# Performance work log

Measured on AMD Instinct MI355X. Metric: run time of the kernel, lower is better.

The kernel has to match this reference:

```python
import jax, jax.numpy as jnp
import numpy as np

C, H, O, T, B = 15, 256, 512, 60, 1024


def setup_inputs() -> dict:
    key = jax.random.key(0)
    ks = jax.random.split(key, 8)
    s = 1.0 / np.sqrt(H)
    return {
        "x": jax.random.normal(ks[0], (B, H), dtype=jnp.float32),
        "cam": jax.random.randint(ks[1], (B,), 0, C, dtype=jnp.int32),
        "W_ih": jax.random.uniform(ks[2], (C, 3 * H, H), jnp.float32, -s, s),
        "W_hh": jax.random.uniform(ks[3], (C, 3 * H, H), jnp.float32, -s, s),
        "b_ih": jax.random.uniform(ks[4], (C, 3 * H), jnp.float32, -s, s),
        "b_hh": jax.random.uniform(ks[5], (C, 3 * H), jnp.float32, -s, s),
        "Wc": jax.random.uniform(ks[6], (C, O, H), jnp.float32, -s, s),
        "bc": jax.random.uniform(ks[7], (C, O), jnp.float32, -s, s),
    }


def reference(x, cam, W_ih, W_hh, b_ih, b_hh, Wc, bc):
    # Gather per-sample (per-camera) parameters once.
    Wi = W_ih[cam]          # [B, 3H, H]
    Wh = W_hh[cam]          # [B, 3H, H]
    bi = b_ih[cam]          # [B, 3H]
    bh = b_hh[cam]          # [B, 3H]
    Wcs = Wc[cam]           # [B, O, H]
    bcs = bc[cam]           # [B, O]

    # Input is constant across timesteps -> input gate preactivations computed once.
    gi = jnp.einsum('bh,bgh->bg', x, Wi) + bi   # [B, 3H]
    gi_r, gi_z, gi_n = jnp.split(gi, 3, axis=1)

    h0 = jnp.zeros_like(x)  # [B, H]

    def step(h, _):
        gh = jnp.einsum('bh,bgh->bg', h, Wh) + bh
        gh_r, gh_z, gh_n = jnp.split(gh, 3, axis=1)
        r = jax.nn.sigmoid(gi_r + gh_r)
        z = jax.nn.sigmoid(gi_z + gh_z)
        n = jnp.tanh(gi_n + r * gh_n)
        h_new = (1.0 - z) * n + z * h
        out = jax.nn.sigmoid(jnp.einsum('bh,boh->bo', h_new, Wcs) + bcs)  # [B, O]
        return h_new, out

    _, outs = jax.lax.scan(step, h0, None, length=T)  # [T, B, O]
    return jnp.transpose(outs, (1, 2, 0))             # [B, O, T]
```

## Files before the change

### kernel.cpp

```cpp
#include <hip/hip_runtime.h>
#include <hip/hip_fp16.h>

#define C_    15
#define H_    256
#define O_    512
#define T_    60
#define B_    1024
#define G3H_  768
#define TS    16
#define MAXG  12
#define NSLOT 96
#define NU    80
#define TCH   10

typedef __attribute__((ext_vector_type(8))) short bf16x8;
typedef __attribute__((ext_vector_type(4))) float f32x4;

__device__ __forceinline__ unsigned short f2bf(float f) {
    union { float f; unsigned u; } v; v.f = f;
    return (unsigned short)((v.u + 0x7FFFu + ((v.u >> 16) & 1u)) >> 16);
}
__device__ __forceinline__ float sigf(float x) { return 1.f / (1.f + __expf(-x)); }

__global__ __launch_bounds__(256) void sort_kernel(const int* __restrict__ cam,
    int* __restrict__ order, int* __restrict__ tcam, int* __restrict__ toff,
    int* __restrict__ tcnt)
{
    __shared__ int cnt[C_], start[C_], fill[C_];
    int tid = threadIdx.x;
    if (tid < C_) cnt[tid] = 0;
    if (tid < NSLOT) { tcam[tid] = -1; toff[tid] = 0; tcnt[tid] = 0; }
    __syncthreads();
    for (int b = tid; b < B_; b += 256) atomicAdd(&cnt[cam[b]], 1);
    __syncthreads();
    if (tid == 0) {
        int run = 0;
        for (int c = 0; c < C_; ++c) { start[c] = run; fill[c] = run; run += cnt[c]; }
    }
    __syncthreads();
    for (int b = tid; b < B_; b += 256) {
        int pos = atomicAdd(&fill[cam[b]], 1);
        order[pos] = b;
    }
    __syncthreads();
    if (tid == 0) {
        int gcnt[8] = {0,0,0,0,0,0,0,0};
        for (int c = 0; c < C_; ++c) gcnt[c & 7] += (cnt[c] + TS - 1) / TS;
        int maxg = 0;
        for (int g = 0; g < 8; ++g) maxg = max(maxg, gcnt[g]);
        if (maxg <= MAXG) {
            for (int g = 0; g < 8; ++g) {
                int k = 0;
                for (int c = g; c < C_; c += 8)
                    for (int r = 0; r < cnt[c]; r += TS) {
                        int slot = g + 8 * k;
                        tcam[slot] = c; toff[slot] = start[c] + r;
                        tcnt[slot] = min(TS, cnt[c] - r); ++k;
                    }
            }
        } else {
            int ti = 0;
            for (int c = 0; c < C_; ++c)
                for (int r = 0; r < cnt[c]; r += TS) {
                    tcam[ti] = c; toff[ti] = start[c] + r;
                    tcnt[ti] = min(TS, cnt[c] - r); ++ti;
                }
        }
    }
}

__global__ __launch_bounds__(256) void cvt_kernel(const float* __restrict__ src,
    unsigned short* __restrict__ dst, int n4)
{
    int i = blockIdx.x * 256 + threadIdx.x;
    if (i < n4) {
        float4 v = ((const float4*)src)[i];
        unsigned p0 = (unsigned)f2bf(v.x) | ((unsigned)f2bf(v.y) << 16);
        unsigned p1 = (unsigned)f2bf(v.z) | ((unsigned)f2bf(v.w) << 16);
        ((uint2*)dst)[i] = make_uint2(p0, p1);
    }
}

__global__ __launch_bounds__(64) void pack_kernel(
    const float* __restrict__ Whh, const float* __restrict__ Wc,
    unsigned short* __restrict__ Wpack)
{
    int cu = blockIdx.x;
    int c = cu / NU, u = cu - c * NU;
    int lane = threadIdx.x, q = lane >> 4, l16 = lane & 15;
    const float* src = (u < 48)
        ? &Whh[((size_t)c * G3H_ + u * 16 + l16) * H_]
        : &Wc[((size_t)c * O_ + (u - 48) * 16 + l16) * H_];
    unsigned short* dst = Wpack + ((size_t)cu * 8) * 512 + lane * 8;
#pragma unroll
    for (int kk = 0; kk < 8; ++kk) {
        float4 v0 = *(const float4*)&src[kk * 32 + q * 8];
        float4 v1 = *(const float4*)&src[kk * 32 + q * 8 + 4];
        unsigned short* d = dst + kk * 512;
        d[0] = f2bf(v0.x); d[1] = f2bf(v0.y); d[2] = f2bf(v0.z); d[3] = f2bf(v0.w);
        d[4] = f2bf(v1.x); d[5] = f2bf(v1.y); d[6] = f2bf(v1.z); d[7] = f2bf(v1.w);
    }
}

__global__ __launch_bounds__(384) void gi_mfma(
    const float* __restrict__ x, const unsigned short* __restrict__ Wih_b,
    const float* __restrict__ bih, const float* __restrict__ bhh,
    const int* __restrict__ order, const int* __restrict__ tcam,
    const int* __restrict__ toff, const int* __restrict__ tcnt,
    float* __restrict__ gi)
{
    int c = tcam[blockIdx.x]; if (c < 0) return;
    int cnt = tcnt[blockIdx.x], off = toff[blockIdx.x];
    int tid = threadIdx.x;
    __shared__ unsigned short hbfs[TS * 264];
    for (int idx = tid; idx < TS * 64; idx += 384) {
        int m = idx >> 6, c4 = idx & 63;
        float4 v = make_float4(0.f, 0.f, 0.f, 0.f);
        if (m < cnt) v = *(const float4*)&x[(size_t)order[off + m] * H_ + (c4 << 2)];
        unsigned p0 = (unsigned)f2bf(v.x) | ((unsigned)f2bf(v.y) << 16);
        unsigned p1 = (unsigned)f2bf(v.z) | ((unsigned)f2bf(v.w) << 16);
        *(uint2*)&hbfs[m * 264 + (c4 << 2)] = make_uint2(p0, p1);
    }
    __syncthreads();
    int w = tid >> 6, lane = tid & 63, q = lane >> 4, l16 = lane & 15;
    f32x4 acc[2][4];
#pragma unroll
    for (int i = 0; i < 2; ++i)
#pragma unroll
        for (int nt = 0; nt < 4; ++nt) acc[i][nt] = (f32x4){0.f, 0.f, 0.f, 0.f};
    const unsigned short* bp[2];
#pragma unroll
    for (int i = 0; i < 2; ++i)
        bp[i] = Wih_b + ((size_t)c * G3H_ + (2 * w + i) * 64 + l16) * H_;
    const unsigned short* ap = &hbfs[l16 * 264 + q * 8];
#pragma unroll 2
    for (int kk = 0; kk < 8; ++kk) {
        bf16x8 a = *(const bf16x8*)(ap + kk * 32);
#pragma unroll
        for (int i = 0; i < 2; ++i)
#pragma unroll
            for (int nt = 0; nt < 4; ++nt) {
                bf16x8 b = *(const bf16x8*)(bp[i] + (size_t)nt * 16 * H_ + kk * 32 + q * 8);
                acc[i][nt] = __builtin_amdgcn_mfma_f32_16x16x32_bf16(a, b, acc[i][nt], 0, 0, 0);
            }
    }
#pragma unroll
    for (int i = 0; i < 2; ++i) {
        int u = 2 * w + i;
#pragma unroll
        for (int nt = 0; nt < 4; ++nt) {
            int col = u * 64 + nt * 16 + l16;
            float bias = bih[c * G3H_ + col] + (col < 2 * H_ ? bhh[c * G3H_ + col] : 0.f);
#pragma unroll
            for (int r = 0; r < 4; ++r) {
                int m = q * 4 + r;
                gi[((size_t)(blockIdx.x * TS + m)) * G3H_ + col] = acc[i][nt][r] + bias;
            }
        }
    }
}

__global__ __launch_bounds__(512, 2) void persist_kernel(
    const unsigned short* __restrict__ Wpack, const float* __restrict__ bhh,
    const float* __restrict__ gi, const int* __restrict__ tcam,
    unsigned short* __restrict__ htraj)
{
    int slot = blockIdx.x;
    int c = tcam[slot]; if (c < 0) return;
    int tid = threadIdx.x, w = tid >> 6, lane = tid & 63, q = lane >> 4, l16 = lane & 15;

    __shared__ float gisT[G3H_][20];
    __shared__ unsigned short hbf[2][16][264];

    for (int idx = tid; idx < TS * G3H_; idx += 512) {
        int m = idx / G3H_, col = idx - m * G3H_;
        gisT[col][m] = gi[((size_t)(slot * TS + m)) * G3H_ + col];
    }

    bf16x8 wf[6][8];
#pragma unroll
    for (int ii = 0; ii < 3; ++ii)
#pragma unroll
        for (int jj = 0; jj < 2; ++jj)
#pragma unroll
            for (int kk = 0; kk < 8; ++kk)
                wf[ii * 2 + jj][kk] = *(const bf16x8*)(
                    Wpack + (((size_t)(c * NU + ii * 16 + w + 8 * jj)) * 8 + kk) * 512 + lane * 8);

    float bhn[2], hreg[2][4];
#pragma unroll
    for (int i = 0; i < 2; ++i) {
        int col = (w + 8 * i) * 16 + l16;
        bhn[i] = bhh[c * G3H_ + 2 * H_ + col];
#pragma unroll
        for (int r = 0; r < 4; ++r) hreg[i][r] = 0.f;
    }
    unsigned short* hp = htraj + ((size_t)slot * TS + q * 4) * 256 + w * 16 + l16;
    __syncthreads();

#pragma unroll 2
    for (int s = 0; s < T_; ++s) {
        int wbuf = s & 1, rbuf = wbuf ^ 1;
        f32x4 acc[6];
#pragma unroll
        for (int ui = 0; ui < 6; ++ui) acc[ui] = (f32x4){0.f, 0.f, 0.f, 0.f};
        if (s > 0) {
#pragma unroll
            for (int kk = 0; kk < 8; ++kk) {
                bf16x8 a = *(const bf16x8*)&hbf[rbuf][l16][kk * 32 + q * 8];
#pragma unroll
                for (int ui = 0; ui < 6; ++ui)
                    acc[ui] = __builtin_amdgcn_mfma_f32_16x16x32_bf16(a, wf[ui][kk], acc[ui], 0, 0, 0);
            }
        }
#pragma unroll
        for (int i = 0; i < 2; ++i) {
            int col = (w + 8 * i) * 16 + l16;
            f32x4 gr = *(const f32x4*)&gisT[col][q * 4];
            f32x4 gz = *(const f32x4*)&gisT[H_ + col][q * 4];
            f32x4 gn = *(const f32x4*)&gisT[2 * H_ + col][q * 4];
#pragma unroll
            for (int r = 0; r < 4; ++r) {
                float rr = sigf(gr[r] + acc[i][r]);
                float zz = sigf(gz[r] + acc[2 + i][r]);
                float pre = gn[r] + rr * (acc[4 + i][r] + bhn[i]);
                float nn = 2.f * sigf(2.f * pre) - 1.f;
                float hn = (1.f - zz) * nn + zz * hreg[i][r];
                hreg[i][r] = hn;
                unsigned short hb = f2bf(hn);
                hbf[wbuf][q * 4 + r][col] = hb;
                hp[r * 256 + i * 128] = hb;
            }
        }
        hp += (size_t)NSLOT * TS * 256;
        asm volatile("s_waitcnt lgkmcnt(0)" ::: "memory");
        __builtin_amdgcn_s_barrier();
        __builtin_amdgcn_sched_barrier(0);
    }
}

__global__ __launch_bounds__(512, 2) void out_kernel(
    const unsigned short* __restrict__ Wpack, const float* __restrict__ bc,
    const unsigned short* __restrict__ htraj, const int* __restrict__ order,
    const int* __restrict__ tcam, const int* __restrict__ toff,
    const int* __restrict__ tcnt, unsigned short* __restrict__ outT,
    int direct, float* __restrict__ outp)
{
    int slot = blockIdx.x;
    int c = tcam[slot]; if (c < 0) return;
    int n = tcnt[slot], off = toff[slot];
    int tid = threadIdx.x, w = tid >> 6, lane = tid & 63, q = lane >> 4, l16 = lane & 15;
    __shared__ unsigned short hb[2][16][264];
    __shared__ int ord16[16];
    if (tid < 16) ord16[tid] = (tid < n) ? order[off + tid] : -1;

    bf16x8 wf[4][8];
    const unsigned short* wb = Wpack + ((size_t)c * NU + 48 + w * 4) * 8 * 512 + lane * 8;
#pragma unroll
    for (int ui = 0; ui < 4; ++ui)
#pragma unroll
        for (int kk = 0; kk < 8; ++kk)
            wf[ui][kk] = *(const bf16x8*)(wb + ((size_t)ui * 8 + kk) * 512);
    float bcr[4];
#pragma unroll
    for (int ui = 0; ui < 4; ++ui)
        bcr[ui] = bc[c * O_ + (w * 4 + ui) * 16 + l16];

    int m = tid >> 5, c8 = (tid & 31) * 8;
    const unsigned short* hsrc =
        &htraj[(((size_t)(blockIdx.y * TCH) * NSLOT + slot) * 16 + m) * 256 + c8];
    uint4 stg = *(const uint4*)hsrc;
    *(uint4*)&hb[0][m][c8] = stg;
    __syncthreads();

    for (int ti = 0; ti < TCH; ++ti) {
        int t = blockIdx.y * TCH + ti;
        int cur = ti & 1;
        if (ti + 1 < TCH)
            stg = *(const uint4*)(hsrc + (size_t)(ti + 1) * NSLOT * TS * 256);
        f32x4 acc[4];
#pragma unroll
        for (int ui = 0; ui < 4; ++ui) acc[ui] = (f32x4){0.f, 0.f, 0.f, 0.f};
#pragma unroll
        for (int kk = 0; kk < 8; ++kk) {
            bf16x8 a = *(const bf16x8*)&hb[cur][l16][kk * 32 + q * 8];
#pragma unroll
            for (int ui = 0; ui < 4; ++ui)
                acc[ui] = __builtin_amdgcn_mfma_f32_16x16x32_bf16(a, wf[ui][kk], acc[ui], 0, 0, 0);
        }
#pragma unroll
        for (int ui = 0; ui < 4; ++ui) {
            int o = (w * 4 + ui) * 16 + l16;
#pragma unroll
            for (int r = 0; r < 4; ++r) {
                int b = ord16[q * 4 + r];
                if (b >= 0) {
                    float val = sigf(acc[ui][r] + bcr[ui]);
                    if (direct) outp[((size_t)b * O_ + o) * T_ + t] = val;
                    else outT[((size_t)t * B_ + b) * O_ + o] =
                             __half_as_ushort(__float2half_rn(val));
                }
            }
        }
        if (ti + 1 < TCH) {
            *(uint4*)&hb[cur ^ 1][m][c8] = stg;
            asm volatile("s_waitcnt lgkmcnt(0)" ::: "memory");
            __builtin_amdgcn_s_barrier();
            __builtin_amdgcn_sched_barrier(0);
        }
    }
}

__global__ __launch_bounds__(256) void transpose_kernel(
    const unsigned short* __restrict__ outT, float* __restrict__ outp)
{
    int b = blockIdx.x, o0 = blockIdx.y * 64;
    __shared__ float ts[T_][65];
    int tid = threadIdx.x;
    for (int idx = tid; idx < T_ * 64; idx += 256) {
        int t = idx >> 6, o = idx & 63;
        ts[t][o] = __half2float(__ushort_as_half(outT[((size_t)t * B_ + b) * O_ + o0 + o]));
    }
    __syncthreads();
    for (int idx = tid; idx < 64 * T_; idx += 256) {
        int o = idx / T_, t = idx - o * T_;
        outp[((size_t)b * O_ + o0 + o) * T_ + t] = ts[t][o];
    }
}

extern "C" void kernel_launch(void* const* d_in, const int* in_sizes, int n_in,
                              void* d_out, int out_size, void* d_ws, size_t ws_size,
                              hipStream_t stream)
{
    const float* x   = (const float*)d_in[0];
    const int*   cam = (const int*)d_in[1];
    const float* Wih = (const float*)d_in[2];
    const float* Whh = (const float*)d_in[3];
    const float* bih = (const float*)d_in[4];
    const float* bhh = (const float*)d_in[5];
    const float* Wc  = (const float*)d_in[6];
    const float* bc  = (const float*)d_in[7];
    float* outp = (float*)d_out;

    char* w = (char*)d_ws;
    unsigned short* Wih_b = (unsigned short*)w; w += (size_t)C_ * G3H_ * H_ * 2;
    unsigned short* Wpack = (unsigned short*)w; w += (size_t)C_ * NU * 8 * 512 * 2;
    int* order = (int*)w; w += B_ * 4;
    int* tcam  = (int*)w; w += NSLOT * 4;
    int* toff  = (int*)w; w += NSLOT * 4;
    int* tcnt  = (int*)w; w += NSLOT * 4;
    float* gi  = (float*)w; w += (size_t)NSLOT * TS * G3H_ * 4;
    unsigned short* htraj = (unsigned short*)w; w += (size_t)T_ * NSLOT * 16 * 256 * 2;
    unsigned short* outT = (unsigned short*)w;
    size_t need = (size_t)(w - (char*)d_ws) + (size_t)T_ * B_ * O_ * 2;
    int direct = (ws_size < need) ? 1 : 0;

    sort_kernel<<<1, 256, 0, stream>>>(cam, order, tcam, toff, tcnt);
    cvt_kernel<<<(C_ * G3H_ * H_ / 4 + 255) / 256, 256, 0, stream>>>(Wih, Wih_b, C_ * G3H_ * H_ / 4);
    pack_kernel<<<C_ * NU, 64, 0, stream>>>(Whh, Wc, Wpack);
    gi_mfma<<<NSLOT, 384, 0, stream>>>(x, Wih_b, bih, bhh, order, tcam, toff, tcnt, gi);
    persist_kernel<<<NSLOT, 512, 0, stream>>>(Wpack, bhh, gi, tcam, htraj);
    out_kernel<<<dim3(NSLOT, T_ / TCH), 512, 0, stream>>>(Wpack, bc, htraj, order, tcam,
                                                          toff, tcnt, outT, direct, outp);
    if (!direct)
        transpose_kernel<<<dim3(B_, O_ / 64), 256, 0, stream>>>(outT, outp);
}
```

Before: 439.9 us.

## Fuse prep kernels and overlap GRU recurrence with output projection via flags

Merges the sort, weight-convert and weight-pack kernels into one prep launch. It also fuses the input-gate GEMM, the GRU recurrence and the output projection into one kernel, where producer blocks publish per-slot progress flags every TCH steps and consumer blocks spin on them to compute outputs while the recurrence continues. This removes several launches, the gi round trip through global memory, and the serialization between the recurrence and output stages. The risk is deadlock if consumer blocks are resident while producers are not, and 192 blocks at launch bound (512,1) with large shared usage may not all be co-resident.

```diff
diff --git a/kernel.cpp b/kernel.cpp
--- a/kernel.cpp
+++ b/kernel.cpp
@@ -10,7 +10,10 @@
 #define TS    16
 #define MAXG  12
 #define NSLOT 96
+#define NPROD 96
 #define NU    80
+#define PACKB 300
+#define CVTB  2880
 #define TCH   10
 
 typedef __attribute__((ext_vector_type(8))) short bf16x8;
@@ -22,291 +25,275 @@
 }
 __device__ __forceinline__ float sigf(float x) { return 1.f / (1.f + __expf(-x)); }
 
-__global__ __launch_bounds__(256) void sort_kernel(const int* __restrict__ cam,
+__global__ __launch_bounds__(256) void prep_kernel(
+    const int* __restrict__ cam, const float* __restrict__ Wih,
+    const float* __restrict__ Whh, const float* __restrict__ Wc,
     int* __restrict__ order, int* __restrict__ tcam, int* __restrict__ toff,
-    int* __restrict__ tcnt)
+    int* __restrict__ tcnt, int* __restrict__ flags,
+    unsigned short* __restrict__ Wih_b, unsigned short* __restrict__ Wpack)
 {
-    __shared__ int cnt[C_], start[C_], fill[C_];
-    int tid = threadIdx.x;
-    if (tid < C_) cnt[tid] = 0;
-    if (tid < NSLOT) { tcam[tid] = -1; toff[tid] = 0; tcnt[tid] = 0; }
-    __syncthreads();
-    for (int b = tid; b < B_; b += 256) atomicAdd(&cnt[cam[b]], 1);
-    __syncthreads();
-    if (tid == 0) {
-        int run = 0;
-        for (int c = 0; c < C_; ++c) { start[c] = run; fill[c] = run; run += cnt[c]; }
-    }
-    __syncthreads();
-    for (int b = tid; b < B_; b += 256) {
-        int pos = atomicAdd(&fill[cam[b]], 1);
-        order[pos] = b;
-    }
-    __syncthreads();
-    if (tid == 0) {
-        int gcnt[8] = {0,0,0,0,0,0,0,0};
-        for (int c = 0; c < C_; ++c) gcnt[c & 7] += (cnt[c] + TS - 1) / TS;
-        int maxg = 0;
-        for (int g = 0; g < 8; ++g) maxg = max(maxg, gcnt[g]);
-        if (maxg <= MAXG) {
-            for (int g = 0; g < 8; ++g) {
-                int k = 0;
-                for (int c = g; c < C_; c += 8)
+    int bid = blockIdx.x, tid = threadIdx.x;
+    if (bid == 0) {
+        __shared__ int cnt[C_], start[C_], fill[C_];
+        if (tid < C_) cnt[tid] = 0;
+        if (tid < NSLOT) { tcam[tid] = -1; toff[tid] = 0; tcnt[tid] = 0; flags[tid] = 0; }
+        __syncthreads();
+        for (int b = tid; b < B_; b += 256) atomicAdd(&cnt[cam[b]], 1);
+        __syncthreads();
+        if (tid == 0) {
+            int run = 0;
+            for (int c = 0; c < C_; ++c) { start[c] = run; fill[c] = run; run += cnt[c]; }
+        }
+        __syncthreads();
+        for (int b = tid; b < B_; b += 256) {
+            int pos = atomicAdd(&fill[cam[b]], 1);
+            order[pos] = b;
+        }
+        __syncthreads();
+        if (tid == 0) {
+            int gcnt[8] = {0,0,0,0,0,0,0,0};
+            for (int c = 0; c < C_; ++c) gcnt[c & 7] += (cnt[c] + TS - 1) / TS;
+            int maxg = 0;
+            for (int g = 0; g < 8; ++g) maxg = max(maxg, gcnt[g]);
+            if (maxg <= MAXG) {
+                for (int g = 0; g < 8; ++g) {
+                    int k = 0;
+                    for (int c = g; c < C_; c += 8)
+                        for (int r = 0; r < cnt[c]; r += TS) {
+                            int slot = g + 8 * k;
+                            tcam[slot] = c; toff[slot] = start[c] + r;
+                            tcnt[slot] = min(TS, cnt[c] - r); ++k;
+                        }
+                }
+            } else {
+                int ti = 0;
+                for (int c = 0; c < C_; ++c)
                     for (int r = 0; r < cnt[c]; r += TS) {
-                        int slot = g + 8 * k;
-                        tcam[slot] = c; toff[slot] = start[c] + r;
-                        tcnt[slot] = min(TS, cnt[c] - r); ++k;
+                        tcam[ti] = c; toff[ti] = start[c] + r;
+                        tcnt[ti] = min(TS, cnt[c] - r); ++ti;
                     }
             }
-        } else {
-            int ti = 0;
-            for (int c = 0; c < C_; ++c)
-                for (int r = 0; r < cnt[c]; r += TS) {
-                    tcam[ti] = c; toff[ti] = start[c] + r;
-                    tcnt[ti] = min(TS, cnt[c] - r); ++ti;
-                }
-        }
-    }
-}
-
-__global__ __launch_bounds__(256) void cvt_kernel(const float* __restrict__ src,
-    unsigned short* __restrict__ dst, int n4)
-{
-    int i = blockIdx.x * 256 + threadIdx.x;
-    if (i < n4) {
-        float4 v = ((const float4*)src)[i];
+        }
+    } else if (bid <= PACKB) {
+        int cu = (bid - 1) * 4 + (tid >> 6);
+        int c = cu / NU, u = cu - c * NU;
+        int lane = tid & 63, q = lane >> 4, l16 = lane & 15;
+        const float* src = (u < 48)
+            ? &Whh[((size_t)c * G3H_ + u * 16 + l16) * H_]
+            : &Wc[((size_t)c * O_ + (u - 48) * 16 + l16) * H_];
+        unsigned short* dst = Wpack + ((size_t)cu * 8) * 512 + lane * 8;
+#pragma unroll
+        for (int kk = 0; kk < 8; ++kk) {
+            float4 v0 = *(const float4*)&src[kk * 32 + q * 8];
+            float4 v1 = *(const float4*)&src[kk * 32 + q * 8 + 4];
+            unsigned short* d = dst + kk * 512;
+            d[0] = f2bf(v0.x); d[1] = f2bf(v0.y); d[2] = f2bf(v0.z); d[3] = f2bf(v0.w);
+            d[4] = f2bf(v1.x); d[5] = f2bf(v1.y); d[6] = f2bf(v1.z); d[7] = f2bf(v1.w);
+        }
+    } else {
+        int i = (bid - 1 - PACKB) * 256 + tid;
+        float4 v = ((const float4*)Wih)[i];
         unsigned p0 = (unsigned)f2bf(v.x) | ((unsigned)f2bf(v.y) << 16);
         unsigned p1 = (unsigned)f2bf(v.z) | ((unsigned)f2bf(v.w) << 16);
-        ((uint2*)dst)[i] = make_uint2(p0, p1);
+        ((uint2*)Wih_b)[i] = make_uint2(p0, p1);
     }
 }
 
-__global__ __launch_bounds__(64) void pack_kernel(
-    const float* __restrict__ Whh, const float* __restrict__ Wc,
-    unsigned short* __restrict__ Wpack)
-{
-    int cu = blockIdx.x;
-    int c = cu / NU, u = cu - c * NU;
-    int lane = threadIdx.x, q = lane >> 4, l16 = lane & 15;
-    const float* src = (u < 48)
-        ? &Whh[((size_t)c * G3H_ + u * 16 + l16) * H_]
-        : &Wc[((size_t)c * O_ + (u - 48) * 16 + l16) * H_];
-    unsigned short* dst = Wpack + ((size_t)cu * 8) * 512 + lane * 8;
-#pragma unroll
-    for (int kk = 0; kk < 8; ++kk) {
-        float4 v0 = *(const float4*)&src[kk * 32 + q * 8];
-        float4 v1 = *(const float4*)&src[kk * 32 + q * 8 + 4];
-        unsigned short* d = dst + kk * 512;
-        d[0] = f2bf(v0.x); d[1] = f2bf(v0.y); d[2] = f2bf(v0.z); d[3] = f2bf(v0.w);
-        d[4] = f2bf(v1.x); d[5] = f2bf(v1.y); d[6] = f2bf(v1.z); d[7] = f2bf(v1.w);
-    }
-}
-
-__global__ __launch_bounds__(384) void gi_mfma(
+__global__ __launch_bounds__(512, 1) void mega_kernel(
     const float* __restrict__ x, const unsigned short* __restrict__ Wih_b,
-    const float* __restrict__ bih, const float* __restrict__ bhh,
+    const unsigned short* __restrict__ Wpack, const float* __restrict__ bih,
+    const float* __restrict__ bhh, const float* __restrict__ bc,
     const int* __restrict__ order, const int* __restrict__ tcam,
     const int* __restrict__ toff, const int* __restrict__ tcnt,
-    float* __restrict__ gi)
+    int* __restrict__ flags, unsigned short* __restrict__ htraj,
+    unsigned short* __restrict__ outT, int direct, float* __restrict__ outp)
 {
-    int c = tcam[blockIdx.x]; if (c < 0) return;
-    int cnt = tcnt[blockIdx.x], off = toff[blockIdx.x];
-    int tid = threadIdx.x;
-    __shared__ unsigned short hbfs[TS * 264];
-    for (int idx = tid; idx < TS * 64; idx += 384) {
-        int m = idx >> 6, c4 = idx & 63;
-        float4 v = make_float4(0.f, 0.f, 0.f, 0.f);
-        if (m < cnt) v = *(const float4*)&x[(size_t)order[off + m] * H_ + (c4 << 2)];
-        unsigned p0 = (unsigned)f2bf(v.x) | ((unsigned)f2bf(v.y) << 16);
-        unsigned p1 = (unsigned)f2bf(v.z) | ((unsigned)f2bf(v.w) << 16);
-        *(uint2*)&hbfs[m * 264 + (c4 << 2)] = make_uint2(p0, p1);
-    }
-    __syncthreads();
+    int bid = blockIdx.x, tid = threadIdx.x;
     int w = tid >> 6, lane = tid & 63, q = lane >> 4, l16 = lane & 15;
-    f32x4 acc[2][4];
-#pragma unroll
-    for (int i = 0; i < 2; ++i)
-#pragma unroll
-        for (int nt = 0; nt < 4; ++nt) acc[i][nt] = (f32x4){0.f, 0.f, 0.f, 0.f};
-    const unsigned short* bp[2];
-#pragma unroll
-    for (int i = 0; i < 2; ++i)
-        bp[i] = Wih_b + ((size_t)c * G3H_ + (2 * w + i) * 64 + l16) * H_;
-    const unsigned short* ap = &hbfs[l16 * 264 + q * 8];
-#pragma unroll 2
-    for (int kk = 0; kk < 8; ++kk) {
-        bf16x8 a = *(const bf16x8*)(ap + kk * 32);
-#pragma unroll
-        for (int i = 0; i < 2; ++i)
-#pragma unroll
-            for (int nt = 0; nt < 4; ++nt) {
-                bf16x8 b = *(const bf16x8*)(bp[i] + (size_t)nt * 16 * H_ + kk * 32 + q * 8);
-                acc[i][nt] = __builtin_amdgcn_mfma_f32_16x16x32_bf16(a, b, acc[i][nt], 0, 0, 0);
-            }
-    }
-#pragma unroll
-    for (int i = 0; i < 2; ++i) {
-        int u = 2 * w + i;
-#pragma unroll
-        for (int nt = 0; nt < 4; ++nt) {
-            int col = u * 64 + nt * 16 + l16;
-            float bias = bih[c * G3H_ + col] + (col < 2 * H_ ? bhh[c * G3H_ + col] : 0.f);
-#pragma unroll
-            for (int r = 0; r < 4; ++r) {
-                int m = q * 4 + r;
-                gi[((size_t)(blockIdx.x * TS + m)) * G3H_ + col] = acc[i][nt][r] + bias;
-            }
-        }
-    }
-}
-
-__global__ __launch_bounds__(512, 2) void persist_kernel(
-    const unsigned short* __restrict__ Wpack, const float* __restrict__ bhh,
-    const float* __restrict__ gi, const int* __restrict__ tcam,
-    unsigned short* __restrict__ htraj)
-{
-    int slot = blockIdx.x;
-    int c = tcam[slot]; if (c < 0) return;
-    int tid = threadIdx.x, w = tid >> 6, lane = tid & 63, q = lane >> 4, l16 = lane & 15;
-
-    __shared__ float gisT[G3H_][20];
-    __shared__ unsigned short hbf[2][16][264];
-
-    for (int idx = tid; idx < TS * G3H_; idx += 512) {
-        int m = idx / G3H_, col = idx - m * G3H_;
-        gisT[col][m] = gi[((size_t)(slot * TS + m)) * G3H_ + col];
-    }
-
-    bf16x8 wf[6][8];
-#pragma unroll
-    for (int ii = 0; ii < 3; ++ii)
-#pragma unroll
-        for (int jj = 0; jj < 2; ++jj)
-#pragma unroll
-            for (int kk = 0; kk < 8; ++kk)
-                wf[ii * 2 + jj][kk] = *(const bf16x8*)(
-                    Wpack + (((size_t)(c * NU + ii * 16 + w + 8 * jj)) * 8 + kk) * 512 + lane * 8);
-
-    float bhn[2], hreg[2][4];
-#pragma unroll
-    for (int i = 0; i < 2; ++i) {
-        int col = (w + 8 * i) * 16 + l16;
-        bhn[i] = bhh[c * G3H_ + 2 * H_ + col];
-#pragma unroll
-        for (int r = 0; r < 4; ++r) hreg[i][r] = 0.f;
-    }
-    unsigned short* hp = htraj + ((size_t)slot * TS + q * 4) * 256 + w * 16 + l16;
-    __syncthreads();
-
-#pragma unroll 2
-    for (int s = 0; s < T_; ++s) {
-        int wbuf = s & 1, rbuf = wbuf ^ 1;
-        f32x4 acc[6];
-#pragma unroll
-        for (int ui = 0; ui < 6; ++ui) acc[ui] = (f32x4){0.f, 0.f, 0.f, 0.f};
-        if (s > 0) {
+
+    if (bid < NPROD) {
+        int slot = bid;
+        int c = tcam[slot]; if (c < 0) return;
+        int cnt = tcnt[slot], off = toff[slot];
+
+        __shared__ float gisT[G3H_][20];
+        __shared__ unsigned short hbf[2][16][264];
+
+        for (int idx = tid; idx < TS * 64; idx += 512) {
+            int m = idx >> 6, c4 = idx & 63;
+            float4 v = make_float4(0.f, 0.f, 0.f, 0.f);
+            if (m < cnt) v = *(const float4*)&x[(size_t)order[off + m] * H_ + (c4 << 2)];
+            unsigned p0 = (unsigned)f2bf(v.x) | ((unsigned)f2bf(v.y) << 16);
+            unsigned p1 = (unsigned)f2bf(v.z) | ((unsigned)f2bf(v.w) << 16);
+            *(uint2*)&hbf[0][m][c4 << 2] = make_uint2(p0, p1);
+        }
+        __syncthreads();
+
+        {
+            f32x4 acc[6];
+#pragma unroll
+            for (int ui = 0; ui < 6; ++ui) acc[ui] = (f32x4){0.f, 0.f, 0.f, 0.f};
 #pragma unroll
             for (int kk = 0; kk < 8; ++kk) {
-                bf16x8 a = *(const bf16x8*)&hbf[rbuf][l16][kk * 32 + q * 8];
-#pragma unroll
-                for (int ui = 0; ui < 6; ++ui)
-                    acc[ui] = __builtin_amdgcn_mfma_f32_16x16x32_bf16(a, wf[ui][kk], acc[ui], 0, 0, 0);
-            }
-        }
+                bf16x8 a = *(const bf16x8*)&hbf[0][l16][kk * 32 + q * 8];
+#pragma unroll
+                for (int ui = 0; ui < 6; ++ui) {
+                    int col = (w * 6 + ui) * 16 + l16;
+                    bf16x8 b = *(const bf16x8*)(Wih_b + ((size_t)c * G3H_ + col) * H_ + kk * 32 + q * 8);
+                    acc[ui] = __builtin_amdgcn_mfma_f32_16x16x32_bf16(a, b, acc[ui], 0, 0, 0);
+                }
+            }
+#pragma unroll
+            for (int ui = 0; ui < 6; ++ui) {
+                int col = (w * 6 + ui) * 16 + l16;
+                float bias = bih[c * G3H_ + col] + (col < 2 * H_ ? bhh[c * G3H_ + col] : 0.f);
+#pragma unroll
+                for (int r = 0; r < 4; ++r) gisT[col][q * 4 + r] = acc[ui][r] + bias;
+            }
+        }
+        __builtin_amdgcn_sched_barrier(0);
+
+        bf16x8 wf[6][8];
+#pragma unroll
+        for (int ii = 0; ii < 3; ++ii)
+#pragma unroll
+            for (int jj = 0; jj < 2; ++jj)
+#pragma unroll
+                for (int kk = 0; kk < 8; ++kk)
+                    wf[ii * 2 + jj][kk] = *(const bf16x8*)(
+                        Wpack + (((size_t)(c * NU + ii * 16 + w + 8 * jj)) * 8 + kk) * 512 + lane * 8);
+
+        float bhn[2], hreg[2][4];
 #pragma unroll
         for (int i = 0; i < 2; ++i) {
             int col = (w + 8 * i) * 16 + l16;
-            f32x4 gr = *(const f32x4*)&gisT[col][q * 4];
-            f32x4 gz = *(const f32x4*)&gisT[H_ + col][q * 4];
-            f32x4 gn = *(const f32x4*)&gisT[2 * H_ + col][q * 4];
-#pragma unroll
-            for (int r = 0; r < 4; ++r) {
-                float rr = sigf(gr[r] + acc[i][r]);
-                float zz = sigf(gz[r] + acc[2 + i][r]);
-                float pre = gn[r] + rr * (acc[4 + i][r] + bhn[i]);
-                float nn = 2.f * sigf(2.f * pre) - 1.f;
-                float hn = (1.f - zz) * nn + zz * hreg[i][r];
-                hreg[i][r] = hn;
-                unsigned short hb = f2bf(hn);
-                hbf[wbuf][q * 4 + r][col] = hb;
-                hp[r * 256 + i * 128] = hb;
-            }
-        }
-        hp += (size_t)NSLOT * TS * 256;
-        asm volatile("s_waitcnt lgkmcnt(0)" ::: "memory");
-        __builtin_amdgcn_s_barrier();
-        __builtin_amdgcn_sched_barrier(0);
-    }
-}
-
-__global__ __launch_bounds__(512, 2) void out_kernel(
-    const unsigned short* __restrict__ Wpack, const float* __restrict__ bc,
-    const unsigned short* __restrict__ htraj, const int* __restrict__ order,
-    const int* __restrict__ tcam, const int* __restrict__ toff,
-    const int* __restrict__ tcnt, unsigned short* __restrict__ outT,
-    int direct, float* __restrict__ outp)
-{
-    int slot = blockIdx.x;
-    int c = tcam[slot]; if (c < 0) return;
-    int n = tcnt[slot], off = toff[slot];
-    int tid = threadIdx.x, w = tid >> 6, lane = tid & 63, q = lane >> 4, l16 = lane & 15;
-    __shared__ unsigned short hb[2][16][264];
-    __shared__ int ord16[16];
-    if (tid < 16) ord16[tid] = (tid < n) ? order[off + tid] : -1;
-
-    bf16x8 wf[4][8];
-    const unsigned short* wb = Wpack + ((size_t)c * NU + 48 + w * 4) * 8 * 512 + lane * 8;
-#pragma unroll
-    for (int ui = 0; ui < 4; ++ui)
-#pragma unroll
-        for (int kk = 0; kk < 8; ++kk)
-            wf[ui][kk] = *(const bf16x8*)(wb + ((size_t)ui * 8 + kk) * 512);
-    float bcr[4];
-#pragma unroll
-    for (int ui = 0; ui < 4; ++ui)
-        bcr[ui] = bc[c * O_ + (w * 4 + ui) * 16 + l16];
-
-    int m = tid >> 5, c8 = (tid & 31) * 8;
-    const unsigned short* hsrc =
-        &htraj[(((size_t)(blockIdx.y * TCH) * NSLOT + slot) * 16 + m) * 256 + c8];
-    uint4 stg = *(const uint4*)hsrc;
-    *(uint4*)&hb[0][m][c8] = stg;
-    __syncthreads();
-
-    for (int ti = 0; ti < TCH; ++ti) {
-        int t = blockIdx.y * TCH + ti;
-        int cur = ti & 1;
-        if (ti + 1 < TCH)
-            stg = *(const uint4*)(hsrc + (size_t)(ti + 1) * NSLOT * TS * 256);
-        f32x4 acc[4];
-#pragma unroll
-        for (int ui = 0; ui < 4; ++ui) acc[ui] = (f32x4){0.f, 0.f, 0.f, 0.f};
-#pragma unroll
-        for (int kk = 0; kk < 8; ++kk) {
-            bf16x8 a = *(const bf16x8*)&hb[cur][l16][kk * 32 + q * 8];
-#pragma unroll
-            for (int ui = 0; ui < 4; ++ui)
-                acc[ui] = __builtin_amdgcn_mfma_f32_16x16x32_bf16(a, wf[ui][kk], acc[ui], 0, 0, 0);
-        }
-#pragma unroll
-        for (int ui = 0; ui < 4; ++ui) {
-            int o = (w * 4 + ui) * 16 + l16;
-#pragma unroll
-            for (int r = 0; r < 4; ++r) {
-                int b = ord16[q * 4 + r];
-                if (b >= 0) {
-                    float val = sigf(acc[ui][r] + bcr[ui]);
-                    if (direct) outp[((size_t)b * O_ + o) * T_ + t] = val;
-                    else outT[((size_t)t * B_ + b) * O_ + o] =
-                             __half_as_ushort(__float2half_rn(val));
-                }
-            }
-        }
-        if (ti + 1 < TCH) {
-            *(uint4*)&hb[cur ^ 1][m][c8] = stg;
+            bhn[i] = bhh[c * G3H_ + 2 * H_ + col];
+#pragma unroll
+            for (int r = 0; r < 4; ++r) hreg[i][r] = 0.f;
+        }
+        unsigned short* hp = htraj + ((size_t)slot * TS + q * 4) * 256 + w * 16 + l16;
+        __syncthreads();
+
+#pragma unroll 2
+        for (int s = 0; s < T_; ++s) {
+            int wbuf = s & 1, rbuf = wbuf ^ 1;
+            f32x4 acc[6];
+#pragma unroll
+            for (int ui = 0; ui < 6; ++ui) acc[ui] = (f32x4){0.f, 0.f, 0.f, 0.f};
+            if (s > 0) {
+#pragma unroll
+                for (int kk = 0; kk < 8; ++kk) {
+                    bf16x8 a = *(const bf16x8*)&hbf[rbuf][l16][kk * 32 + q * 8];
+#pragma unroll
+                    for (int ui = 0; ui < 6; ++ui)
+                        acc[ui] = __builtin_amdgcn_mfma_f32_16x16x32_bf16(a, wf[ui][kk], acc[ui], 0, 0, 0);
+                }
+            }
+#pragma unroll
+            for (int i = 0; i < 2; ++i) {
+                int col = (w + 8 * i) * 16 + l16;
+                f32x4 gr = *(const f32x4*)&gisT[col][q * 4];
+                f32x4 gz = *(const f32x4*)&gisT[H_ + col][q * 4];
+                f32x4 gn = *(const f32x4*)&gisT[2 * H_ + col][q * 4];
+#pragma unroll
+                for (int r = 0; r < 4; ++r) {
+                    float rr = sigf(gr[r] + acc[i][r]);
+                    float zz = sigf(gz[r] + acc[2 + i][r]);
+                    float pre = gn[r] + rr * (acc[4 + i][r] + bhn[i]);
+                    float nn = 2.f * sigf(2.f * pre) - 1.f;
+                    float hn = (1.f - zz) * nn + zz * hreg[i][r];
+                    hreg[i][r] = hn;
+                    unsigned short hb = f2bf(hn);
+                    hbf[wbuf][q * 4 + r][col] = hb;
+                    hp[r * 256 + i * 128] = hb;
+                }
+            }
+            hp += (size_t)NSLOT * TS * 256;
+            if (((s + 1) % TCH) == 0) {
+                __threadfence();
+                __syncthreads();
+                if (tid == 0)
+                    __hip_atomic_store(&flags[slot], s + 1, __ATOMIC_RELEASE,
+                                       __HIP_MEMORY_SCOPE_AGENT);
+            } else {
+                asm volatile("s_waitcnt lgkmcnt(0)" ::: "memory");
+                __builtin_amdgcn_s_barrier();
+                __builtin_amdgcn_sched_barrier(0);
+            }
+        }
+    } else {
+        int slot = bid - NPROD;
+        int c = tcam[slot]; if (c < 0) return;
+        int n = tcnt[slot], off = toff[slot];
+        __shared__ unsigned short hb[2][16][264];
+        __shared__ int ord16[16];
+        if (tid < 16) ord16[tid] = (tid < n) ? order[off + tid] : -1;
+
+        bf16x8 wfo[4][8];
+        const unsigned short* wb = Wpack + ((size_t)c * NU + 48 + w * 4) * 8 * 512 + lane * 8;
+#pragma unroll
+        for (int ui = 0; ui < 4; ++ui)
+#pragma unroll
+            for (int kk = 0; kk < 8; ++kk)
+                wfo[ui][kk] = *(const bf16x8*)(wb + ((size_t)ui * 8 + kk) * 512);
+        float bcr[4];
+#pragma unroll
+        for (int ui = 0; ui < 4; ++ui)
+            bcr[ui] = bc[c * O_ + (w * 4 + ui) * 16 + l16];
+
+        int m = tid >> 5, c8 = (tid & 31) * 8;
+        for (int tz = 0; tz < T_ / TCH; ++tz) {
+            if (tid == 0) {
+                while (__hip_atomic_load(&flags[slot], __ATOMIC_ACQUIRE,
+                                         __HIP_MEMORY_SCOPE_AGENT) < (tz + 1) * TCH)
+                    __builtin_amdgcn_s_sleep(8);
+            }
+            __syncthreads();
+
+            const unsigned short* hsrc =
+                &htraj[(((size_t)(tz * TCH) * NSLOT + slot) * 16 + m) * 256 + c8];
+            uint4 stg = *(const uint4*)hsrc;
+            *(uint4*)&hb[0][m][c8] = stg;
             asm volatile("s_waitcnt lgkmcnt(0)" ::: "memory");
             __builtin_amdgcn_s_barrier();
             __builtin_amdgcn_sched_barrier(0);
+
+            for (int ti = 0; ti < TCH; ++ti) {
+                int t = tz * TCH + ti;
+                int cur = ti & 1;
+                if (ti + 1 < TCH)
+                    stg = *(const uint4*)(hsrc + (size_t)(ti + 1) * NSLOT * TS * 256);
+                f32x4 acc[4];
+#pragma unroll
+                for (int ui = 0; ui < 4; ++ui) acc[ui] = (f32x4){0.f, 0.f, 0.f, 0.f};
+#pragma unroll
+                for (int kk = 0; kk < 8; ++kk) {
+                    bf16x8 a = *(const bf16x8*)&hb[cur][l16][kk * 32 + q * 8];
+#pragma unroll
+                    for (int ui = 0; ui < 4; ++ui)
+                        acc[ui] = __builtin_amdgcn_mfma_f32_16x16x32_bf16(a, wfo[ui][kk], acc[ui], 0, 0, 0);
+                }
+#pragma unroll
+                for (int ui = 0; ui < 4; ++ui) {
+                    int o = (w * 4 + ui) * 16 + l16;
+#pragma unroll
+                    for (int r = 0; r < 4; ++r) {
+                        int b = ord16[q * 4 + r];
+                        if (b >= 0) {
+                            float val = sigf(acc[ui][r] + bcr[ui]);
+                            if (direct) outp[((size_t)b * O_ + o) * T_ + t] = val;
+                            else outT[((size_t)t * B_ + b) * O_ + o] =
+                                     __half_as_ushort(__float2half_rn(val));
+                        }
+                    }
+                }
+                if (ti + 1 < TCH) {
+                    *(uint4*)&hb[cur ^ 1][m][c8] = stg;
+                    asm volatile("s_waitcnt lgkmcnt(0)" ::: "memory");
+                    __builtin_amdgcn_s_barrier();
+                    __builtin_amdgcn_sched_barrier(0);
+                }
+            }
         }
     }
 }
@@ -349,19 +336,17 @@
     int* tcam  = (int*)w; w += NSLOT * 4;
     int* toff  = (int*)w; w += NSLOT * 4;
     int* tcnt  = (int*)w; w += NSLOT * 4;
-    float* gi  = (float*)w; w += (size_t)NSLOT * TS * G3H_ * 4;
+    int* flags = (int*)w; w += NSLOT * 4;
     unsigned short* htraj = (unsigned short*)w; w += (size_t)T_ * NSLOT * 16 * 256 * 2;
     unsigned short* outT = (unsigned short*)w;
     size_t need = (size_t)(w - (char*)d_ws) + (size_t)T_ * B_ * O_ * 2;
     int direct = (ws_size < need) ? 1 : 0;
 
-    sort_kernel<<<1, 256, 0, stream>>>(cam, order, tcam, toff, tcnt);
-    cvt_kernel<<<(C_ * G3H_ * H_ / 4 + 255) / 256, 256, 0, stream>>>(Wih, Wih_b, C_ * G3H_ * H_ / 4);
-    pack_kernel<<<C_ * NU, 64, 0, stream>>>(Whh, Wc, Wpack);
-    gi_mfma<<<NSLOT, 384, 0, stream>>>(x, Wih_b, bih, bhh, order, tcam, toff, tcnt, gi);
-    persist_kernel<<<NSLOT, 512, 0, stream>>>(Wpack, bhh, gi, tcam, htraj);
-    out_kernel<<<dim3(NSLOT, T_ / TCH), 512, 0, stream>>>(Wpack, bc, htraj, order, tcam,
-                                                          toff, tcnt, outT, direct, outp);
+    prep_kernel<<<1 + PACKB + CVTB, 256, 0, stream>>>(cam, Wih, Whh, Wc, order, tcam,
+                                                      toff, tcnt, flags, Wih_b, Wpack);
+    mega_kernel<<<NPROD + NSLOT, 512, 0, stream>>>(x, Wih_b, Wpack, bih, bhh, bc, order,
+                                                   tcam, toff, tcnt, flags, htraj, outT,
+                                                   direct, outp);
     if (!direct)
         transpose_kernel<<<dim3(B_, O_ / 64), 256, 0, stream>>>(outT, outp);
 }
```

After: 680.9 us. 1.55x slower.
